# Performance work log

Measured on AMD Instinct MI355X. Metric: run time of the kernel, lower is better.

The kernel has to match this reference:

```python
import jax, jax.numpy as jnp
import numpy as np

N = 2000  # nodes per graph (hardcoded in the original module)


def gatv2(x, src, dst, edge_attr, Wl, Wr, We, att, b):
    """PyG GATv2Conv (concat=True, negative_slope=0.2, edge_dim) forward.
    x: [N, Fin]; src/dst: [E]; edge_attr: [E, 2]; att: [H, C]. Returns [N, H*C]."""
    n = x.shape[0]
    H, C = att.shape
    xl = (x @ Wl).reshape(n, H, C)            # messages from source nodes
    xr = (x @ Wr).reshape(n, H, C)            # target-node term
    ee = (edge_attr @ We).reshape(-1, H, C)   # edge feature term
    m = jax.nn.leaky_relu(xl[src] + xr[dst] + ee, 0.2)
    logits = jnp.einsum('ehc,hc->eh', m, att)           # [E, H]
    lmax = jax.ops.segment_max(logits, dst, num_segments=n)
    p = jnp.exp(logits - lmax[dst])
    denom = jax.ops.segment_sum(p, dst, num_segments=n)
    alpha = p / (denom[dst] + 1e-16)                    # scatter-softmax over in-edges
    out = jax.ops.segment_sum(alpha[:, :, None] * xl[src], dst, num_segments=n)
    return out.reshape(n, H * C) + b


def setup_inputs() -> dict:
    key = jax.random.key(0)
    ks = jax.random.split(key, 32)
    B, T, F, E = 4, 10, 8, 16000
    s = 0.05
    d = {
        'x': jax.random.normal(ks[0], (B, T, N, F), jnp.float32),
        'edge_index': jax.random.randint(ks[1], (2, E), 0, N, jnp.int32),
        'edge_attr': jax.random.normal(ks[2], (E, 2), jnp.float32),
        'w_l0': s * jax.random.normal(ks[3], (8, 128)),
        'w_r0': s * jax.random.normal(ks[4], (8, 128)),
        'w_e0': s * jax.random.normal(ks[5], (2, 128)),
        'att0': s * jax.random.normal(ks[6], (4, 32)),
        'b0': s * jax.random.normal(ks[7], (128,)),
        'w_l1': s * jax.random.normal(ks[8], (128, 128)),
        'w_r1': s * jax.random.normal(ks[9], (128, 128)),
        'w_e1': s * jax.random.normal(ks[10], (2, 128)),
        'att1': s * jax.random.normal(ks[11], (4, 32)),
        'b1': s * jax.random.normal(ks[12], (128,)),
        'w_l2': s * jax.random.normal(ks[13], (128, 32)),
        'w_r2': s * jax.random.normal(ks[14], (128, 32)),
        'w_e2': s * jax.random.normal(ks[15], (2, 32)),
        'att2': s * jax.random.normal(ks[16], (4, 8)),
        'b2': s * jax.random.normal(ks[17], (32,)),
        'w_ih': s * jax.random.normal(ks[18], (1024, 64000)),
        'w_hh': s * jax.random.normal(ks[19], (1024, 256)),
        'b_ih': s * jax.random.normal(ks[20], (1024,)),
        'b_hh': s * jax.random.normal(ks[21], (1024,)),
        'fc1_w': s * jax.random.normal(ks[22], (256, 512)),
        'fc1_b': s * jax.random.normal(ks[23], (512,)),
        'fc2_w': s * jax.random.normal(ks[24], (512, 1)),
        'fc2_b': s * jax.random.normal(ks[25], (1,)),
    }
    return d


def reference(x, edge_index, edge_attr, w_l0, w_r0, w_e0, att0, b0,
              w_l1, w_r1, w_e1, att1, b1, w_l2, w_r2, w_e2, att2, b2,
              w_ih, w_hh, b_ih, b_hh, fc1_w, fc1_b, fc2_w, fc2_b):
    B, T = x.shape[0], x.shape[1]
    # PyG GATv2Conv add_self_loops=True with fill_value='mean' for edge_attr
    loop = jnp.arange(N, dtype=edge_index.dtype)
    src = jnp.concatenate([edge_index[0], loop])
    dst = jnp.concatenate([edge_index[1], loop])
    ea = jnp.concatenate([edge_attr, jnp.broadcast_to(edge_attr.mean(0), (N, 2))], axis=0)

    def gat_stack(xt):  # [N, F] -> [N*32] flattened embedding
        h = jax.nn.relu(gatv2(xt, src, dst, ea, w_l0, w_r0, w_e0, att0, b0))
        h = jax.nn.relu(gatv2(h, src, dst, ea, w_l1, w_r1, w_e1, att1, b1))
        h = jax.nn.relu(gatv2(h, src, dst, ea, w_l2, w_r2, w_e2, att2, b2))
        return h.reshape(-1)

    emb = jax.vmap(jax.vmap(gat_stack))(x)  # [B, T, 64000]

    # single-layer LSTM (torch gate order: i, f, g, o)
    Hh = w_hh.shape[1]
    def step(carry, xt):
        h, c = carry
        g = xt @ w_ih.T + h @ w_hh.T + (b_ih + b_hh)
        i, f, gg, o = jnp.split(g, 4, axis=-1)
        c = jax.nn.sigmoid(f) * c + jax.nn.sigmoid(i) * jnp.tanh(gg)
        h = jax.nn.sigmoid(o) * jnp.tanh(c)
        return (h, c), h
    h0 = jnp.zeros((B, Hh), emb.dtype)
    (_, _), hs = jax.lax.scan(step, (h0, h0), jnp.swapaxes(emb, 0, 1))  # hs: [T, B, Hh]

    last = jax.nn.relu(hs[-1])                       # relu(lstm_out)[:, -1, :]
    hid = jax.nn.relu(last @ fc1_w + fc1_b)          # (dropout=0 -> identity)
    return hid @ fc2_w + fc2_b                       # [B, 1]
```

## Files before the change

kernel.cpp:

```cpp
#include <hip/hip_runtime.h>
#include <hip/hip_bf16.h>
#include <math.h>

typedef __hip_bfloat16 bf16;
typedef __attribute__((ext_vector_type(8))) short short8;
typedef __attribute__((ext_vector_type(4))) float f32x4;

#define NNODES 2000
#define NEDGE_IN 16000
#define NEDGE 18000
#define NGRAPH 40

__device__ __forceinline__ float bf2f(bf16 v){ return __bfloat162float(v); }
__device__ __forceinline__ bf16 f2bf(float v){ return __float2bfloat16(v); }
__device__ __forceinline__ short bfbits(float v){ bf16 t = __float2bfloat16(v); return *reinterpret_cast<short*>(&t); }

__global__ __launch_bounds__(256) void k_setup(const float* __restrict__ ea, float* __restrict__ mean_ea,
                        const float* __restrict__ whh, unsigned* __restrict__ whhT2,
                        const float* __restrict__ w1a, const float* __restrict__ w1b,
                        const float* __restrict__ w2a, const float* __restrict__ w2b,
                        bf16* __restrict__ b1a, bf16* __restrict__ b1b,
                        bf16* __restrict__ b2a, bf16* __restrict__ b2b,
                        int* __restrict__ cnt, int* __restrict__ cursor, float* __restrict__ gates){
  int bb = blockIdx.x, tid = threadIdx.x;
  if (bb == 0){
    __shared__ float s0l[256], s1l[256];
    float s0=0.f, s1=0.f;
    for (int e = tid; e < NEDGE_IN; e += 256){ s0 += ea[2*e]; s1 += ea[2*e+1]; }
    s0l[tid]=s0; s1l[tid]=s1; __syncthreads();
    for (int d=128; d>=1; d>>=1){
      if (tid < d){ s0l[tid]+=s0l[tid+d]; s1l[tid]+=s1l[tid+d]; }
      __syncthreads();
    }
    if (tid==0){ mean_ea[0]=s0l[0]/(float)NEDGE_IN; mean_ea[1]=s1l[0]/(float)NEDGE_IN; }
  } else if (bb < 513){
    int idx = (bb-1)*256 + tid;
    int j = idx >> 7, kp = idx & 127;
    unsigned ulo = (unsigned)(unsigned short)bfbits(whh[j*256 + 2*kp]);
    unsigned uhi = (unsigned)(unsigned short)bfbits(whh[j*256 + 2*kp + 1]);
    whhT2[kp*1024 + j] = (uhi<<16) | ulo;
  } else if (bb < 673){
    int idx = (bb-513)*256 + tid;
    const float* src; bf16* dst; int n, local;
    if (idx < 16384){ src=w1a; dst=b1a; n=128; local=idx; }
    else if (idx < 32768){ src=w1b; dst=b1b; n=128; local=idx-16384; }
    else if (idx < 36864){ src=w2a; dst=b2a; n=32; local=idx-32768; }
    else { src=w2b; dst=b2b; n=32; local=idx-36864; }
    int k = local / n, c = local % n;
    dst[c*128 + k] = f2bf(src[local]);
  } else {
    int idx = (bb-673)*256 + tid;
    if (idx < 2000) cnt[idx] = 0;
    else if (idx < 4000) cursor[idx-2000] = 0;
    else if (idx < 44960) gates[idx-4000] = 0.f;
  }
}

__global__ void k_count(const int* __restrict__ ei, int* __restrict__ cnt){
  int e = blockIdx.x*256 + threadIdx.x;
  if (e >= NEDGE) return;
  int d = (e < NEDGE_IN) ? ei[NEDGE_IN + e] : (e - NEDGE_IN);
  atomicAdd(&cnt[d], 1);
}

__global__ void k_scan(const int* __restrict__ cnt, int* __restrict__ off){
  __shared__ int s[2048];
  int lane = threadIdx.x;
  for (int i = lane; i < 2048; i += 64) s[i] = (i < NNODES) ? cnt[i] : 0;
  __syncthreads();
  int base = lane*32, run = 0;
  for (int j=0;j<32;j++){ int t = s[base+j]; s[base+j] = run; run += t; }
  int x = run;
  for (int d=1; d<64; d<<=1){ int y = __shfl_up(x, d); if (lane >= d) x += y; }
  int chunkOff = x - run;
  for (int j=0;j<32;j++){ int idx = base+j; if (idx <= NNODES) off[idx] = chunkOff + s[idx]; }
}

__global__ void k_scatter(const int* __restrict__ ei, const int* __restrict__ off,
                          int* __restrict__ cursor, const float* __restrict__ ea,
                          const float* __restrict__ mean_ea,
                          int* __restrict__ csr_src, float2* __restrict__ eaP){
  int e = blockIdx.x*256 + threadIdx.x;
  if (e >= NEDGE) return;
  int d, sn; float2 a;
  if (e < NEDGE_IN){ sn = ei[e]; d = ei[NEDGE_IN+e]; a = ((const float2*)ea)[e]; }
  else { sn = e-NEDGE_IN; d = sn; a.x = mean_ea[0]; a.y = mean_ea[1]; }
  int p = off[d] + atomicAdd(&cursor[d], 1);
  csr_src[p] = sn;
  eaP[p] = a;
}

__global__ __launch_bounds__(256) void k_gemm0(const float* __restrict__ X, const float* __restrict__ Wa,
                                               const float* __restrict__ Wb,
                                               bf16* __restrict__ Ya, bf16* __restrict__ Yb){
  __shared__ float Ws[2*8*128];
  for (int i = threadIdx.x; i < 8*128; i += 256){ Ws[i] = Wa[i]; Ws[1024+i] = Wb[i]; }
  __syncthreads();
  int j  = threadIdx.x % 128;
  int rg = threadIdx.x / 128;
  size_t m0 = (size_t)blockIdx.x*8 + (size_t)rg*4;
  const float* x0 = X + m0*8;
  float a0=0.f,a1=0.f,a2=0.f,a3=0.f, b0=0.f,b1=0.f,b2=0.f,b3=0.f;
  #pragma unroll
  for (int k=0;k<8;k++){
    float wa = Ws[k*128 + j], wb = Ws[1024 + k*128 + j];
    float x_0 = x0[k], x_1 = x0[8+k], x_2 = x0[16+k], x_3 = x0[24+k];
    a0 += x_0*wa; a1 += x_1*wa; a2 += x_2*wa; a3 += x_3*wa;
    b0 += x_0*wb; b1 += x_1*wb; b2 += x_2*wb; b3 += x_3*wb;
  }
  bf16* ya = Ya + m0*128 + j;
  bf16* yb = Yb + m0*128 + j;
  ya[0]=f2bf(a0); ya[128]=f2bf(a1); ya[256]=f2bf(a2); ya[384]=f2bf(a3);
  yb[0]=f2bf(b0); yb[128]=f2bf(b1); yb[256]=f2bf(b2); yb[384]=f2bf(b3);
}

template<int N>
__global__ __launch_bounds__(256) void k_gemm_mf2(const bf16* __restrict__ A, const bf16* __restrict__ BTa,
                                                  const bf16* __restrict__ BTb,
                                                  bf16* __restrict__ Ya, bf16* __restrict__ Yb){
  const int NT = N/16;
  int lane = threadIdx.x & 63, wv = threadIdx.x >> 6;
  size_t m0 = (size_t)blockIdx.x*128 + (size_t)wv*32;
  int r = lane & 15, kg = lane >> 4;
  const f32x4 zero = {0.f,0.f,0.f,0.f};
  f32x4 acca[2][NT], accb[2][NT];
  #pragma unroll
  for (int s=0;s<2;s++)
    #pragma unroll
    for (int t=0;t<NT;t++){ acca[s][t] = zero; accb[s][t] = zero; }
  #pragma unroll
  for (int c=0;c<4;c++){
    short8 a0 = *(const short8*)(A + (m0 + r)*128 + c*32 + kg*8);
    short8 a1 = *(const short8*)(A + (m0 + 16 + r)*128 + c*32 + kg*8);
    #pragma unroll
    for (int t=0;t<NT;t++){
      short8 ba = *(const short8*)(BTa + (size_t)(t*16 + r)*128 + c*32 + kg*8);
      short8 bb = *(const short8*)(BTb + (size_t)(t*16 + r)*128 + c*32 + kg*8);
      acca[0][t] = __builtin_amdgcn_mfma_f32_16x16x32_bf16(a0, ba, acca[0][t], 0,0,0);
      acca[1][t] = __builtin_amdgcn_mfma_f32_16x16x32_bf16(a1, ba, acca[1][t], 0,0,0);
      accb[0][t] = __builtin_amdgcn_mfma_f32_16x16x32_bf16(a0, bb, accb[0][t], 0,0,0);
      accb[1][t] = __builtin_amdgcn_mfma_f32_16x16x32_bf16(a1, bb, accb[1][t], 0,0,0);
    }
  }
  #pragma unroll
  for (int s=0;s<2;s++)
    #pragma unroll
    for (int t=0;t<NT;t++){
      size_t row = m0 + s*16 + kg*4;
      int col = t*16 + r;
      #pragma unroll
      for (int i=0;i<4;i++){
        Ya[(row+i)*N + col] = f2bf(acca[s][t][i]);
        Yb[(row+i)*N + col] = f2bf(accb[s][t][i]);
      }
    }
}

template<int H, int C>
__global__ __launch_bounds__(256) void k_edge(const bf16* __restrict__ XL, const bf16* __restrict__ XR,
                                              const float2* __restrict__ eaP, const int* __restrict__ off,
                                              const int* __restrict__ csr_src, const float* __restrict__ att,
                                              const float* __restrict__ We, const float* __restrict__ bias,
                                              bf16* __restrict__ Hout){
  const int HC = H*C;
  const int LPN = HC/2;
  const int NPW = 64/LPN;
  const int NPB = 4*NPW;
  int tid = threadIdx.x;
  int lane = tid & 63, wv = tid >> 6;
  int ln = lane % LPN;
  int n  = blockIdx.x*NPB + wv*NPW + lane/LPN;
  int g  = blockIdx.y;
  int c0 = 2*ln;
  size_t gbase = (size_t)g*NNODES*HC;
  const unsigned* XLu = (const unsigned*)(XL + gbase);
  unsigned xru = ((const unsigned*)(XR + gbase))[n*LPN + ln];
  float xr0 = __uint_as_float(xru<<16);
  float xr1 = __uint_as_float(xru & 0xffff0000u);
  float av0 = att[c0], av1 = att[c0+1];
  float w00 = We[c0], w01 = We[c0+1];
  float w10 = We[HC+c0], w11 = We[HC+c0+1];
  float srun = 0.f, acc0 = 0.f, acc1 = 0.f;
  int p0 = off[n], p1 = off[n+1];
  int p = p0;
  for (; p+2 <= p1; p += 2){
    int uA = csr_src[p], uB = csr_src[p+1];
    float2 eA = eaP[p], eB = eaP[p+1];
    unsigned xlA = XLu[uA*LPN + ln];
    unsigned xlB = XLu[uB*LPN + ln];
    float xa0 = __uint_as_float(xlA<<16), xa1 = __uint_as_float(xlA & 0xffff0000u);
    float xb0 = __uint_as_float(xlB<<16), xb1 = __uint_as_float(xlB & 0xffff0000u);
    float sa0 = xa0 + fmaf(eA.x,w00, fmaf(eA.y,w10, xr0));
    float sa1 = xa1 + fmaf(eA.x,w01, fmaf(eA.y,w11, xr1));
    float sb0 = xb0 + fmaf(eB.x,w00, fmaf(eB.y,w10, xr0));
    float sb1 = xb1 + fmaf(eB.x,w01, fmaf(eB.y,w11, xr1));
    float ma0 = sa0>0.f?sa0:0.2f*sa0, ma1 = sa1>0.f?sa1:0.2f*sa1;
    float mb0 = sb0>0.f?sb0:0.2f*sb0, mb1 = sb1>0.f?sb1:0.2f*sb1;
    float cA = fmaf(ma0,av0, ma1*av1);
    float cB = fmaf(mb0,av0, mb1*av1);
    #pragma unroll
    for (int d=C/4; d>=1; d>>=1){ cA += __shfl_xor(cA, d); cB += __shfl_xor(cB, d); }
    float peA = __expf(cA), peB = __expf(cB);
    srun += peA + peB;
    acc0 = fmaf(peA, xa0, fmaf(peB, xb0, acc0));
    acc1 = fmaf(peA, xa1, fmaf(peB, xb1, acc1));
  }
  if (p < p1){
    int uA = csr_src[p];
    float2 eA = eaP[p];
    unsigned xlA = XLu[uA*LPN + ln];
    float xa0 = __uint_as_float(xlA<<16), xa1 = __uint_as_float(xlA & 0xffff0000u);
    float sa0 = xa0 + fmaf(eA.x,w00, fmaf(eA.y,w10, xr0));
    float sa1 = xa1 + fmaf(eA.x,w01, fmaf(eA.y,w11, xr1));
    float ma0 = sa0>0.f?sa0:0.2f*sa0, ma1 = sa1>0.f?sa1:0.2f*sa1;
    float cA = fmaf(ma0,av0, ma1*av1);
    #pragma unroll
    for (int d=C/4; d>=1; d>>=1) cA += __shfl_xor(cA, d);
    float peA = __expf(cA);
    srun += peA;
    acc0 = fmaf(peA, xa0, acc0);
    acc1 = fmaf(peA, xa1, acc1);
  }
  float inv = 1.f/(srun + 1e-16f);
  float o0 = fmaf(acc0, inv, bias[c0]);
  float o1 = fmaf(acc1, inv, bias[c0+1]);
  o0 = o0>0.f?o0:0.f; o1 = o1>0.f?o1:0.f;
  unsigned r0 = (unsigned)(unsigned short)bfbits(o0);
  unsigned r1 = (unsigned)(unsigned short)bfbits(o1);
  ((unsigned*)(Hout + gbase))[n*LPN + ln] = (r1<<16) | r0;
}

#define GATES_KS 40
__global__ __launch_bounds__(256) void k_gates_mf(const bf16* __restrict__ emb, const float* __restrict__ wih,
                                                  float* __restrict__ gates){
  const int nk = 2000/GATES_KS;
  int lane = threadIdx.x & 63, wv = threadIdx.x >> 6;
  int r = lane & 15, kg = lane >> 4;
  int j0 = (blockIdx.x*4 + wv)*16;
  int k0 = blockIdx.y*nk*32;
  const f32x4 zero = {0.f,0.f,0.f,0.f};
  f32x4 acc0 = zero, acc1 = zero, acc2 = zero;
  const float* wrow = wih + (size_t)(j0 + r)*64000;
  const bf16*  e0p  = emb + (size_t)r*64000;
  const bf16*  e1p  = emb + (size_t)(16+r)*64000;
  const bf16*  e2p  = emb + (size_t)(32+r)*64000;
  #pragma unroll 2
  for (int s=0; s<nk; ++s){
    int k = k0 + s*32 + kg*8;
    float4 wa = *(const float4*)(wrow + k);
    float4 wb = *(const float4*)(wrow + k + 4);
    short8 bfr;
    bfr[0]=bfbits(wa.x); bfr[1]=bfbits(wa.y); bfr[2]=bfbits(wa.z); bfr[3]=bfbits(wa.w);
    bfr[4]=bfbits(wb.x); bfr[5]=bfbits(wb.y); bfr[6]=bfbits(wb.z); bfr[7]=bfbits(wb.w);
    short8 a0 = *(const short8*)(e0p + k);
    short8 a1 = *(const short8*)(e1p + k);
    short8 a2 = *(const short8*)(e2p + k);
    acc0 = __builtin_amdgcn_mfma_f32_16x16x32_bf16(a0, bfr, acc0, 0,0,0);
    acc1 = __builtin_amdgcn_mfma_f32_16x16x32_bf16(a1, bfr, acc1, 0,0,0);
    acc2 = __builtin_amdgcn_mfma_f32_16x16x32_bf16(a2, bfr, acc2, 0,0,0);
  }
  int col = j0 + r;
  #pragma unroll
  for (int i=0;i<4;i++){
    int row = kg*4 + i;
    atomicAdd(&gates[(size_t)row*1024 + col], acc0[i]);
    atomicAdd(&gates[(size_t)(row+16)*1024 + col], acc1[i]);
    if (row + 32 < 40) atomicAdd(&gates[(size_t)(row+32)*1024 + col], acc2[i]);
  }
}

__global__ __launch_bounds__(1024) void k_lstm10(const float* __restrict__ gates, const unsigned* __restrict__ whhT2,
                                                 const float* __restrict__ bih, const float* __restrict__ bhh,
                                                 float* __restrict__ hst){
  __shared__ float hs[256];
  __shared__ float g[1024];
  int b = blockIdx.x, j = threadIdx.x;
  float c_reg = 0.f;
  if (j < 256) hs[j] = 0.f;
  float bias = bih[j] + bhh[j];
  __syncthreads();
  for (int t=0;t<10;t++){
    float acc = gates[(size_t)(b*10+t)*1024 + j] + bias;
    #pragma unroll 16
    for (int kp=0;kp<128;kp++){
      unsigned u = whhT2[kp*1024 + j];
      float2 h2 = *(const float2*)&hs[2*kp];
      acc = fmaf(__uint_as_float(u<<16), h2.x, acc);
      acc = fmaf(__uint_as_float(u & 0xffff0000u), h2.y, acc);
    }
    g[j] = acc;
    __syncthreads();
    if (j < 256){
      float i_ = g[j], f_ = g[j+256], gg = g[j+512], o_ = g[j+768];
      float si = 1.f/(1.f+__expf(-i_));
      float sf = 1.f/(1.f+__expf(-f_));
      float so = 1.f/(1.f+__expf(-o_));
      c_reg = sf*c_reg + si*tanhf(gg);
      float hn = so*tanhf(c_reg);
      hs[j] = hn;
      if (t==9) hst[b*256+j] = hn;
    }
    __syncthreads();
  }
}

__global__ __launch_bounds__(512) void k_head(const float* __restrict__ hst, const float* __restrict__ fc1w,
                                              const float* __restrict__ fc1b, const float* __restrict__ fc2w,
                                              const float* __restrict__ fc2b, float* __restrict__ out){
  __shared__ float r[512];
  int b = blockIdx.x, j = threadIdx.x;
  float acc = fc1b[j];
  for (int k=0;k<256;k++){
    float l = hst[b*256+k]; l = l>0.f?l:0.f;
    acc += l * fc1w[k*512 + j];
  }
  float hid = acc>0.f?acc:0.f;
  r[j] = hid * fc2w[j];
  __syncthreads();
  for (int d=256; d>=1; d>>=1){ if (j<d) r[j]+=r[j+d]; __syncthreads(); }
  if (j==0) out[b] = r[0] + fc2b[0];
}

extern "C" void kernel_launch(void* const* d_in, const int* in_sizes, int n_in,
                              void* d_out, int out_size, void* d_ws, size_t ws_size,
                              hipStream_t stream){
  const float* x    = (const float*)d_in[0];
  const int*   ei   = (const int*)  d_in[1];
  const float* ea   = (const float*)d_in[2];
  const float* wl0  = (const float*)d_in[3];
  const float* wr0  = (const float*)d_in[4];
  const float* we0  = (const float*)d_in[5];
  const float* att0 = (const float*)d_in[6];
  const float* b0   = (const float*)d_in[7];
  const float* wl1  = (const float*)d_in[8];
  const float* wr1  = (const float*)d_in[9];
  const float* we1  = (const float*)d_in[10];
  const float* att1 = (const float*)d_in[11];
  const float* b1   = (const float*)d_in[12];
  const float* wl2  = (const float*)d_in[13];
  const float* wr2  = (const float*)d_in[14];
  const float* we2  = (const float*)d_in[15];
  const float* att2 = (const float*)d_in[16];
  const float* b2   = (const float*)d_in[17];
  const float* wih  = (const float*)d_in[18];
  const float* whh  = (const float*)d_in[19];
  const float* bih  = (const float*)d_in[20];
  const float* bhh  = (const float*)d_in[21];
  const float* fc1w = (const float*)d_in[22];
  const float* fc1b = (const float*)d_in[23];
  const float* fc2w = (const float*)d_in[24];
  const float* fc2b = (const float*)d_in[25];
  float* out = (float*)d_out;

  char* base = (char*)d_ws; size_t cur = 0;
  auto alloc = [&](size_t bytes)->void*{
    cur = (cur + 255) & ~(size_t)255; void* p = base + cur; cur += bytes; return p;
  };
  float* mean_ea = (float*)alloc(8);
  int*   cnt     = (int*)  alloc((size_t)NNODES*4);
  int*   off     = (int*)  alloc((size_t)(NNODES+1)*4);
  int*   cursor  = (int*)  alloc((size_t)NNODES*4);
  int*   csr_src = (int*)  alloc((size_t)NEDGE*4);
  float2* eaP    = (float2*)alloc((size_t)NEDGE*8);
  bf16*  XL      = (bf16*) alloc((size_t)80000*128*2);
  bf16*  XR      = (bf16*) alloc((size_t)80000*128*2);
  bf16*  HBUF    = (bf16*) alloc((size_t)80000*128*2);
  float* gates   = (float*)alloc((size_t)40*1024*4);
  float* hst     = (float*)alloc(4*256*4);
  unsigned* whhT2= (unsigned*)alloc((size_t)128*1024*4);
  bf16*  bt1a    = (bf16*) alloc((size_t)128*128*2);
  bf16*  bt1b    = (bf16*) alloc((size_t)128*128*2);
  bf16*  bt2a    = (bf16*) alloc((size_t)32*128*2);
  bf16*  bt2b    = (bf16*) alloc((size_t)32*128*2);

  k_setup <<<849,256,0,stream>>>(ea, mean_ea, whh, whhT2, wl1, wr1, wl2, wr2,
                                 bt1a, bt1b, bt2a, bt2b, cnt, cursor, gates);
  k_count   <<<(NEDGE+255)/256,256,0,stream>>>(ei, cnt);
  k_scan    <<<1,64,0,stream>>>(cnt, off);
  k_scatter <<<(NEDGE+255)/256,256,0,stream>>>(ei, off, cursor, ea, mean_ea, csr_src, eaP);

  k_gemm0   <<<10000,256,0,stream>>>(x, wl0, wr0, XL, XR);
  k_edge<4,32> <<<dim3(500,40),256,0,stream>>>(XL,XR,eaP,off,csr_src,att0,we0,b0,HBUF);

  k_gemm_mf2<128> <<<625,256,0,stream>>>(HBUF, bt1a, bt1b, XL, XR);
  k_edge<4,32> <<<dim3(500,40),256,0,stream>>>(XL,XR,eaP,off,csr_src,att1,we1,b1,HBUF);

  k_gemm_mf2<32> <<<625,256,0,stream>>>(HBUF, bt2a, bt2b, XL, XR);
  k_edge<4,8> <<<dim3(125,40),256,0,stream>>>(XL,XR,eaP,off,csr_src,att2,we2,b2,HBUF);

  k_gates_mf<<<dim3(16,GATES_KS),256,0,stream>>>(HBUF, wih, gates);

  k_lstm10<<<4,1024,0,stream>>>(gates, whhT2, bih, bhh, hst);

  k_head<<<4,512,0,stream>>>(hst, fc1w, fc1b, fc2w, fc2b, out);
}
```

Measured before the change: 430.4 us.

## Process all 40 graphs per node in one block for HC=128 edge layers

Adds k_edge_g, where each block handles one destination node and its four waves each cover 10 graphs. The CSR edge index, edge attributes and edge-feature projection are then loaded once per edge and shared across graphs, instead of being reloaded for every graph. The cost is a serial per-edge loop with 10 independent gathers per lane and more registers per thread. Only 2000 blocks are launched instead of 20000, which may reduce occupancy and latency hiding.

Result: faster. 417.7 us (-2.9%).

```diff
diff --git a/kernel.cpp b/kernel.cpp
--- a/kernel.cpp
+++ b/kernel.cpp
@@ -14,6 +14,8 @@
 __device__ __forceinline__ float bf2f(bf16 v){ return __bfloat162float(v); }
 __device__ __forceinline__ bf16 f2bf(float v){ return __float2bfloat16(v); }
 __device__ __forceinline__ short bfbits(float v){ bf16 t = __float2bfloat16(v); return *reinterpret_cast<short*>(&t); }
+__device__ __forceinline__ float blo(unsigned u){ return __uint_as_float(u<<16); }
+__device__ __forceinline__ float bhi(unsigned u){ return __uint_as_float(u & 0xffff0000u); }
 
 __global__ __launch_bounds__(256) void k_setup(const float* __restrict__ ea, float* __restrict__ mean_ea,
                         const float* __restrict__ whh, unsigned* __restrict__ whhT2,
@@ -156,6 +158,69 @@
     }
 }
 
+__global__ __launch_bounds__(256) void k_edge_g(const bf16* __restrict__ XL, const bf16* __restrict__ XR,
+                                                const float2* __restrict__ eaP, const int* __restrict__ off,
+                                                const int* __restrict__ csr_src, const float* __restrict__ att,
+                                                const float* __restrict__ We, const float* __restrict__ bias,
+                                                bf16* __restrict__ Hout){
+  int tid = threadIdx.x;
+  int ln = tid & 63;
+  int gq = tid >> 6;
+  int n  = blockIdx.x;
+  int c0 = 2*ln;
+  float av0 = att[c0], av1 = att[c0+1];
+  float w00 = We[c0], w01 = We[c0+1];
+  float w10 = We[128+c0], w11 = We[128+c0+1];
+  const unsigned* XLu = (const unsigned*)XL;
+  const unsigned* XRu = (const unsigned*)XR;
+  float xr0[10], xr1[10], srun[10], acc0[10], acc1[10];
+  #pragma unroll
+  for (int t=0;t<10;t++){
+    int g = gq*10 + t;
+    unsigned xu = XRu[((size_t)g*NNODES + n)*64 + ln];
+    xr0[t] = blo(xu); xr1[t] = bhi(xu);
+    srun[t]=0.f; acc0[t]=0.f; acc1[t]=0.f;
+  }
+  int p0 = off[n], p1 = off[n+1];
+  for (int p = p0; p < p1; ++p){
+    int u = csr_src[p];
+    float2 e = eaP[p];
+    float ed0 = fmaf(e.x, w00, e.y*w10);
+    float ed1 = fmaf(e.x, w01, e.y*w11);
+    unsigned xl[10];
+    #pragma unroll
+    for (int t=0;t<10;t++){
+      int g = gq*10 + t;
+      xl[t] = XLu[((size_t)g*NNODES + u)*64 + ln];
+    }
+    #pragma unroll
+    for (int t=0;t<10;t++){
+      float x0 = blo(xl[t]), x1 = bhi(xl[t]);
+      float s0 = x0 + xr0[t] + ed0;
+      float s1 = x1 + xr1[t] + ed1;
+      float m0 = s0>0.f?s0:0.2f*s0, m1 = s1>0.f?s1:0.2f*s1;
+      float c = fmaf(m0, av0, m1*av1);
+      #pragma unroll
+      for (int d=8; d>=1; d>>=1) c += __shfl_xor(c, d);
+      float pe = __expf(c);
+      srun[t] += pe;
+      acc0[t] = fmaf(pe, x0, acc0[t]);
+      acc1[t] = fmaf(pe, x1, acc1[t]);
+    }
+  }
+  #pragma unroll
+  for (int t=0;t<10;t++){
+    int g = gq*10 + t;
+    float inv = 1.f/(srun[t] + 1e-16f);
+    float o0 = fmaf(acc0[t], inv, bias[c0]);
+    float o1 = fmaf(acc1[t], inv, bias[c0+1]);
+    o0 = o0>0.f?o0:0.f; o1 = o1>0.f?o1:0.f;
+    unsigned r0 = (unsigned)(unsigned short)bfbits(o0);
+    unsigned r1 = (unsigned)(unsigned short)bfbits(o1);
+    ((unsigned*)Hout)[((size_t)g*NNODES + n)*64 + ln] = (r1<<16) | r0;
+  }
+}
+
 template<int H, int C>
 __global__ __launch_bounds__(256) void k_edge(const bf16* __restrict__ XL, const bf16* __restrict__ XR,
                                               const float2* __restrict__ eaP, const int* __restrict__ off,
@@ -175,8 +240,7 @@
   size_t gbase = (size_t)g*NNODES*HC;
   const unsigned* XLu = (const unsigned*)(XL + gbase);
   unsigned xru = ((const unsigned*)(XR + gbase))[n*LPN + ln];
-  float xr0 = __uint_as_float(xru<<16);
-  float xr1 = __uint_as_float(xru & 0xffff0000u);
+  float xr0 = blo(xru), xr1 = bhi(xru);
   float av0 = att[c0], av1 = att[c0+1];
   float w00 = We[c0], w01 = We[c0+1];
   float w10 = We[HC+c0], w11 = We[HC+c0+1];
@@ -188,8 +252,8 @@
     float2 eA = eaP[p], eB = eaP[p+1];
     unsigned xlA = XLu[uA*LPN + ln];
     unsigned xlB = XLu[uB*LPN + ln];
-    float xa0 = __uint_as_float(xlA<<16), xa1 = __uint_as_float(xlA & 0xffff0000u);
-    float xb0 = __uint_as_float(xlB<<16), xb1 = __uint_as_float(xlB & 0xffff0000u);
+    float xa0 = blo(xlA), xa1 = bhi(xlA);
+    float xb0 = blo(xlB), xb1 = bhi(xlB);
     float sa0 = xa0 + fmaf(eA.x,w00, fmaf(eA.y,w10, xr0));
     float sa1 = xa1 + fmaf(eA.x,w01, fmaf(eA.y,w11, xr1));
     float sb0 = xb0 + fmaf(eB.x,w00, fmaf(eB.y,w10, xr0));
@@ -209,7 +273,7 @@
     int uA = csr_src[p];
     float2 eA = eaP[p];
     unsigned xlA = XLu[uA*LPN + ln];
-    float xa0 = __uint_as_float(xlA<<16), xa1 = __uint_as_float(xlA & 0xffff0000u);
+    float xa0 = blo(xlA), xa1 = bhi(xlA);
     float sa0 = xa0 + fmaf(eA.x,w00, fmaf(eA.y,w10, xr0));
     float sa1 = xa1 + fmaf(eA.x,w01, fmaf(eA.y,w11, xr1));
     float ma0 = sa0>0.f?sa0:0.2f*sa0, ma1 = sa1>0.f?sa1:0.2f*sa1;
@@ -285,8 +349,8 @@
     for (int kp=0;kp<128;kp++){
       unsigned u = whhT2[kp*1024 + j];
       float2 h2 = *(const float2*)&hs[2*kp];
-      acc = fmaf(__uint_as_float(u<<16), h2.x, acc);
-      acc = fmaf(__uint_as_float(u & 0xffff0000u), h2.y, acc);
+      acc = fmaf(blo(u), h2.x, acc);
+      acc = fmaf(bhi(u), h2.y, acc);
     }
     g[j] = acc;
     __syncthreads();
@@ -380,10 +444,10 @@
   k_scatter <<<(NEDGE+255)/256,256,0,stream>>>(ei, off, cursor, ea, mean_ea, csr_src, eaP);
 
   k_gemm0   <<<10000,256,0,stream>>>(x, wl0, wr0, XL, XR);
-  k_edge<4,32> <<<dim3(500,40),256,0,stream>>>(XL,XR,eaP,off,csr_src,att0,we0,b0,HBUF);
+  k_edge_g  <<<NNODES,256,0,stream>>>(XL,XR,eaP,off,csr_src,att0,we0,b0,HBUF);
 
   k_gemm_mf2<128> <<<625,256,0,stream>>>(HBUF, bt1a, bt1b, XL, XR);
-  k_edge<4,32> <<<dim3(500,40),256,0,stream>>>(XL,XR,eaP,off,csr_src,att1,we1,b1,HBUF);
+  k_edge_g  <<<NNODES,256,0,stream>>>(XL,XR,eaP,off,csr_src,att1,we1,b1,HBUF);
 
   k_gemm_mf2<32> <<<625,256,0,stream>>>(HBUF, bt2a, bt2b, XL, XR);
   k_edge<4,8> <<<dim3(125,40),256,0,stream>>>(XL,XR,eaP,off,csr_src,att2,we2,b2,HBUF);
```
